# Optimization experiments

Hardware: AMD Instinct MI355X
Metric: run time of the kernel (lower is better)

Reference implementation:

```python
import jax, jax.numpy as jnp
import numpy as np

N_HEADS = 16

def setup_inputs() -> dict:
    key = jax.random.key(0)
    ks = jax.random.split(key, 8)
    B, S, D = 2, 2048, 2048
    H, hd = N_HEADS, D // N_HEADS
    w_scale = 0.02  # keep pre-softmax logits in a sane range
    return {
        "x": jax.random.normal(ks[0], (B, S, D), jnp.float32),
        "Wq": jax.random.normal(ks[1], (D, D), jnp.float32) * w_scale,
        "bq": jax.random.normal(ks[2], (D,), jnp.float32) * w_scale,
        "Wk": jax.random.normal(ks[3], (D, D), jnp.float32) * w_scale,
        "bk": jax.random.normal(ks[4], (D,), jnp.float32) * w_scale,
        "Wv": jax.random.normal(ks[5], (D, D), jnp.float32) * w_scale,
        "bv": jax.random.normal(ks[6], (D,), jnp.float32) * w_scale,
        "k_cache": jnp.zeros((B, H, S, hd), jnp.float32),
        "v_cache": jnp.zeros((B, H, S, hd), jnp.float32),
        "start_pos": 0,
    }

def reference(x, Wq, bq, Wk, bk, Wv, bv, k_cache, v_cache, start_pos):
    B, S, D = x.shape
    H = N_HEADS
    hd = D // H
    # qkv projections (nn.Linear equivalent)
    q_val = (x @ Wq + bq).reshape(B, H, S, hd)  # faithful .view: pure reshape, NO transpose
    k_val = (x @ Wk + bk).reshape(B, H, S, hd)
    v_val = (x @ Wv + bv).reshape(B, H, S, hd)
    # KV-cache scatter update at input_pos = [start_pos, start_pos+S)
    pos = jnp.arange(S) + start_pos
    k_cache = k_cache.at[:, :, pos].set(k_val)
    v_cache = v_cache.at[:, :, pos].set(v_val)
    L = k_cache.shape[2]
    # QK^T / sqrt(hd)
    scores = jnp.einsum('bhsd,bhld->bhsl', q_val, k_cache) / jnp.sqrt(jnp.asarray(hd, x.dtype))
    # default mask path: triu(ones, diag=1) is the KEEP mask (faithful to source)
    mask = jnp.triu(jnp.ones((S, L), x.dtype), 1)
    scores = scores - 1e9 * (1.0 - mask)
    probs = jax.nn.softmax(scores, axis=-1)
    out = jnp.einsum('bhsl,bhld->bhsd', probs, v_cache)  # [B,H,S,hd]
    return out.reshape(B, S, D)  # faithful .view(B, -1, D)
```

## Files before the change

kernel.cpp:

```cpp
#include <hip/hip_runtime.h>
#include <math.h>

#define BATCH 2
#define SEQ   2048
#define DIM   2048
#define NH    16
#define HD    128
#define MTOT  (BATCH*SEQ)
static constexpr float SCALE = 0.08838834764831845f;


typedef short s8  __attribute__((ext_vector_type(8)));
typedef float f4  __attribute__((ext_vector_type(4)));

__device__ inline unsigned short bf_rn(float f) {
    union { float f; unsigned u; } v; v.f = f;
    unsigned r = v.u + 0x7FFFu + ((v.u >> 16) & 1u);
    return (unsigned short)(r >> 16);
}
__device__ inline float bf_f(unsigned short h) {
    union { float f; unsigned u; } v; v.u = ((unsigned)h) << 16; return v.f;
}

#define GLL(g, l) __builtin_amdgcn_global_load_lds( \
    (const __attribute__((address_space(1))) void*)(g), \
    (__attribute__((address_space(3))) void*)(l), 16, 0, 0)

__global__ __launch_bounds__(256) void convert_x(
    const float* __restrict__ x, unsigned short* __restrict__ xh)
{
    size_t i = ((size_t)blockIdx.x * 256 + threadIdx.x) * 4;
    float4 v = *(const float4*)(x + i);
    float a[4] = {v.x, v.y, v.z, v.w};
    ushort4 h;
    unsigned short* hp = &h.x;
    #pragma unroll
    for (int j = 0; j < 4; ++j) hp[j] = bf_rn(a[j]);
    *(ushort4*)(xh + i) = h;
}

__global__ __launch_bounds__(256) void convert_wT(
    const float* __restrict__ Wq, const float* __restrict__ Wk,
    const float* __restrict__ Wv,
    unsigned short* __restrict__ Wth)
{
    const int z = blockIdx.z;
    const float* W = (z == 0) ? Wq : (z == 1) ? Wk : Wv;
    unsigned short* th = Wth + (size_t)z * DIM * DIM;

    __shared__ unsigned short Th[64][72];

    const int k0 = blockIdx.x * 64;
    const int n0 = blockIdx.y * 64;
    const int tid = threadIdx.x;

    #pragma unroll
    for (int i = 0; i < 4; ++i) {
        int idx = tid + i * 256;
        int kk = idx >> 4, n4 = idx & 15;
        float4 w = *(const float4*)(W + (size_t)(k0 + kk) * DIM + n0 + n4 * 4);
        float a[4] = {w.x, w.y, w.z, w.w};
        #pragma unroll
        for (int j = 0; j < 4; ++j)
            Th[n4 * 4 + j][kk] = bf_rn(a[j]);
    }
    __syncthreads();
    #pragma unroll
    for (int i = 0; i < 2; ++i) {
        int idx = tid + i * 256;
        int nn = idx >> 3, c = idx & 7;
        *(uint4*)(th + (size_t)(n0 + nn) * DIM + k0 + c * 8) =
            *(const uint4*)(&Th[nn][c * 8]);
    }
}

__global__ __launch_bounds__(256) void qkv_mfma_split(
    const unsigned short* __restrict__ xh,
    const unsigned short* __restrict__ Wth,
    const float* __restrict__ bq, const float* __restrict__ bk,
    const float* __restrict__ bv,
    unsigned short* __restrict__ qh_, unsigned short* __restrict__ ql_,
    unsigned short* __restrict__ kh_, unsigned short* __restrict__ vh_)
{
    const int z = blockIdx.z;
    const unsigned short* Bhg = Wth + (size_t)z * DIM * DIM;
    const float* bias = (z == 0) ? bq : (z == 1) ? bk : bv;
    unsigned short* dh = (z == 0) ? qh_ : (z == 1) ? kh_ : vh_;
    unsigned short* dl = (z == 0) ? ql_ : (unsigned short*)nullptr;

    const int bm = blockIdx.x * 128;
    const int bn = blockIdx.y * 128;

    __shared__ unsigned short Ah[128 * 32];
    __shared__ unsigned short Bh[128 * 32];

    const int tid = threadIdx.x;
    const int w = tid >> 6, lane = tid & 63;
    const int wr = w >> 1, wc = w & 1;
    const int lr = lane & 15, lg = lane >> 4;

    const int rA0 = bm + (2 * w + 0) * 16 + (lane >> 2);
    const int rA1 = bm + (2 * w + 1) * 16 + (lane >> 2);
    const int rB0 = bn + (2 * w + 0) * 16 + (lane >> 2);
    const int rB1 = bn + (2 * w + 1) * 16 + (lane >> 2);
    const int kin = (lane & 3) * 8;
    const unsigned short* gah0 = xh + (size_t)rA0 * DIM + kin;
    const unsigned short* gah1 = xh + (size_t)rA1 * DIM + kin;
    const unsigned short* gbh0 = Bhg + (size_t)rB0 * DIM + kin;
    const unsigned short* gbh1 = Bhg + (size_t)rB1 * DIM + kin;
    unsigned short* lah0 = &Ah[(2 * w + 0) * 512];
    unsigned short* lah1 = &Ah[(2 * w + 1) * 512];
    unsigned short* lbh0 = &Bh[(2 * w + 0) * 512];
    unsigned short* lbh1 = &Bh[(2 * w + 1) * 512];

    f4 zero4 = {0.f, 0.f, 0.f, 0.f};
    f4 acc[4][4];
    #pragma unroll
    for (int mi = 0; mi < 4; ++mi)
        #pragma unroll
        for (int ni = 0; ni < 4; ++ni) acc[mi][ni] = zero4;

    const unsigned short* pAh = &Ah[(wr * 64 + lr) * 32 + lg * 8];
    const unsigned short* pBh = &Bh[(wc * 64 + lr) * 32 + lg * 8];

    for (int k0 = 0; k0 < DIM; k0 += 32) {
        GLL(gah0 + k0, lah0); GLL(gah1 + k0, lah1);
        GLL(gbh0 + k0, lbh0); GLL(gbh1 + k0, lbh1);
        __syncthreads();

        s8 fah[4], fbh[4];
        #pragma unroll
        for (int i = 0; i < 4; ++i) {
            fah[i] = *(const s8*)(pAh + i * 512);
            fbh[i] = *(const s8*)(pBh + i * 512);
        }
        #pragma unroll
        for (int mi = 0; mi < 4; ++mi)
            #pragma unroll
            for (int ni = 0; ni < 4; ++ni)
                acc[mi][ni] = __builtin_amdgcn_mfma_f32_16x16x32_bf16(
                    fah[mi], fbh[ni], acc[mi][ni], 0, 0, 0);
        __syncthreads();
    }

    float bv_[4]; int col_[4];
    #pragma unroll
    for (int ni = 0; ni < 4; ++ni) {
        col_[ni] = bn + wc * 64 + ni * 16 + lr;
        bv_[ni] = bias[col_[ni]];
    }
    #pragma unroll
    for (int mi = 0; mi < 4; ++mi)
        #pragma unroll
        for (int ni = 0; ni < 4; ++ni)
            #pragma unroll
            for (int r = 0; r < 4; ++r) {
                int row = bm + wr * 64 + mi * 16 + lg * 4 + r;
                float v = acc[mi][ni][r] + bv_[ni];
                size_t idx = (size_t)row * DIM + col_[ni];
                unsigned short h = bf_rn(v);
                dh[idx] = h;
                if (dl) dl[idx] = bf_rn(v - bf_f(h));
            }
}

__global__ __launch_bounds__(256) void transpose_v(
    const unsigned short* __restrict__ vh, unsigned short* __restrict__ vth)
{
    __shared__ unsigned short T[64][72];
    const int s0 = blockIdx.x * 64;
    const int d0 = blockIdx.y * 64;
    const int bh = blockIdx.z;
    const int tid = threadIdx.x;
    {
        const int r = tid >> 2, cs = tid & 3;
        size_t g = ((size_t)bh * SEQ + s0 + r) * HD + d0 + cs * 16;
        *(uint4*)(&T[r][cs * 16])     = *(const uint4*)(vh + g);
        *(uint4*)(&T[r][cs * 16 + 8]) = *(const uint4*)(vh + g + 8);
    }
    __syncthreads();
    {
        const int d = tid >> 2, ss = tid & 3;
        unsigned short bh_[16];
        #pragma unroll
        for (int j = 0; j < 16; ++j)
            bh_[j] = T[ss * 16 + j][d];
        size_t t = ((size_t)bh * HD + d0 + d) * SEQ + s0 + ss * 16;
        *(uint4*)(vth + t)     = ((const uint4*)bh_)[0];
        *(uint4*)(vth + t + 8) = ((const uint4*)bh_)[1];
    }
}

#define KVBLK 32
#define NT    (SEQ / KVBLK)
#define PSTR  40

__global__ __launch_bounds__(256) void attn_mfma(
    const unsigned short* __restrict__ qh, const unsigned short* __restrict__ ql,
    const unsigned short* __restrict__ kh,
    const unsigned short* __restrict__ vth,
    float* __restrict__ out)
{
    __shared__ unsigned short KhA[KVBLK * HD], KhB[KVBLK * HD];
    __shared__ unsigned short VhA[HD * KVBLK], VhB[HD * KVBLK];
    __shared__ unsigned short Ph[4][32 * PSTR];

    const int bid  = blockIdx.x;
    const int slot = bid >> 8;
    const int idx  = bid & 255;
    const int bh_i = idx >> 3;
    const int j    = idx & 7;
    const int qb   = slot ? (14 - j)
                          : (j == 0 ? 0 : (j == 1 ? 15 : j - 1));
    const int h  = bh_i & 15;
    const int b  = bh_i >> 4;
    const int qs = qb * 128;

    const int tid = threadIdx.x;
    const int w = tid >> 6, lane = tid & 63;
    const int lr = lane & 15, lg = lane >> 4;
    const int q0 = w * 32;

    const size_t hbase = (size_t)(b * NH + h) * SEQ * HD;

    s8 fqh[2][4], fql[2][4];
    #pragma unroll
    for (int mi = 0; mi < 2; ++mi)
        #pragma unroll
        for (int k4 = 0; k4 < 4; ++k4) {
            size_t off = hbase + (size_t)(qs + q0 + mi * 16 + lr) * HD
                       + (size_t)((k4 * 4 + lg) * 8);
            fqh[mi][k4] = *(const s8*)(qh + off);
            fql[mi][k4] = *(const s8*)(ql + off);
        }

    s8 ones;
    #pragma unroll
    for (int i = 0; i < 8; ++i) ones[i] = (short)0x3F80;

    f4 O[2][8], Os[2];
    f4 zero4 = {0.f, 0.f, 0.f, 0.f};
    #pragma unroll
    for (int mi = 0; mi < 2; ++mi) {
        #pragma unroll
        for (int nj = 0; nj < 8; ++nj) O[mi][nj] = zero4;
        Os[mi] = zero4;
    }
    float mrun[2][4];
    #pragma unroll
    for (int mi = 0; mi < 2; ++mi)
        #pragma unroll
        for (int r = 0; r < 4; ++r) mrun[mi][r] = -INFINITY;

    const int kr0 = (2 * w + 0) * 4 + (lane >> 4);
    const int kr1 = (2 * w + 1) * 4 + (lane >> 4);
    const int ks  = lane & 15;
    const int vd0 = (2 * w + 0) * 16 + (lane >> 2);
    const int vd1 = (2 * w + 1) * 16 + (lane >> 2);
    const int vs  = lane & 3;
    const size_t kg0 = hbase + (size_t)kr0 * HD + (size_t)((ks ^ (kr0 & 7)) * 8);
    const size_t kg1 = hbase + (size_t)kr1 * HD + (size_t)((ks ^ (kr1 & 7)) * 8);
    const size_t vg0 = hbase + (size_t)vd0 * SEQ + (size_t)((vs ^ (vd0 & 3)) * 8);
    const size_t vg1 = hbase + (size_t)vd1 * SEQ + (size_t)((vs ^ (vd1 & 3)) * 8);

    const int t0 = (qb == 15) ? 0 : qb * 4;

#define STAGE(T_, KH_, VH_) do {                                             \
        const size_t koff = (size_t)(T_) * KVBLK * HD;                       \
        const int    loff = (T_) * KVBLK;                                    \
        GLL(kh + kg0 + koff, &KH_[(2 * w + 0) * 512]);                       \
        GLL(kh + kg1 + koff, &KH_[(2 * w + 1) * 512]);                       \
        GLL(vth + vg0 + loff, &VH_[(2 * w + 0) * 512]);                      \
        GLL(vth + vg1 + loff, &VH_[(2 * w + 1) * 512]);                      \
    } while (0)

    auto compute = [&](int t, const unsigned short* KH, const unsigned short* VH) {
        const int l0 = t * KVBLK;

        s8 fkh[2][4];
        #pragma unroll
        for (int nj = 0; nj < 2; ++nj) {
            const int n = nj * 16 + lr;
            #pragma unroll
            for (int k4 = 0; k4 < 4; ++k4) {
                const int sl = (k4 * 4 + lg) ^ (n & 7);
                fkh[nj][k4] = *(const s8*)(&KH[n * HD + sl * 8]);
            }
        }
        f4 sc[2][2];
        #pragma unroll
        for (int mi = 0; mi < 2; ++mi)
            #pragma unroll
            for (int nj = 0; nj < 2; ++nj) sc[mi][nj] = zero4;
        #pragma unroll
        for (int k4 = 0; k4 < 4; ++k4)
            #pragma unroll
            for (int mi = 0; mi < 2; ++mi)
                #pragma unroll
                for (int nj = 0; nj < 2; ++nj) {
                    sc[mi][nj] = __builtin_amdgcn_mfma_f32_16x16x32_bf16(
                        fqh[mi][k4], fkh[nj][k4], sc[mi][nj], 0, 0, 0);
                    sc[mi][nj] = __builtin_amdgcn_mfma_f32_16x16x32_bf16(
                        fql[mi][k4], fkh[nj][k4], sc[mi][nj], 0, 0, 0);
                }

        float v0[2][4], v1[2][4];
        bool need = false;
        #pragma unroll
        for (int mi = 0; mi < 2; ++mi)
            #pragma unroll
            for (int r = 0; r < 4; ++r) {
                const int srow = qs + q0 + mi * 16 + lg * 4 + r;
                float a = sc[mi][0][r] * SCALE;
                float c = sc[mi][1][r] * SCALE;
                if (l0 + lr      <= srow) a -= 1e9f;
                if (l0 + 16 + lr <= srow) c -= 1e9f;
                v0[mi][r] = a; v1[mi][r] = c;
                const float lim = mrun[mi][r] + 8.f;
                need = need || (a > lim) || (c > lim);
            }

        if (__any(need)) {
            #pragma unroll
            for (int mi = 0; mi < 2; ++mi)
                #pragma unroll
                for (int r = 0; r < 4; ++r) {
                    float rmax = fmaxf(v0[mi][r], v1[mi][r]);
                    #pragma unroll
                    for (int m_ = 1; m_ < 16; m_ <<= 1)
                        rmax = fmaxf(rmax, __shfl_xor(rmax, m_, 64));
                    const float mnew = fmaxf(mrun[mi][r], rmax);
                    const float corr = __expf(mrun[mi][r] - mnew);
                    mrun[mi][r] = mnew;
                    #pragma unroll
                    for (int nj = 0; nj < 8; ++nj) O[mi][nj][r] *= corr;
                    Os[mi][r] *= corr;
                }
        }

        #pragma unroll
        for (int mi = 0; mi < 2; ++mi)
            #pragma unroll
            for (int r = 0; r < 4; ++r) {
                const float p0 = __expf(v0[mi][r] - mrun[mi][r]);
                const float p1 = __expf(v1[mi][r] - mrun[mi][r]);
                const int q = mi * 16 + lg * 4 + r;
                Ph[w][q * PSTR + lr]      = bf_rn(p0);
                Ph[w][q * PSTR + 16 + lr] = bf_rn(p1);
            }

        s8 fph[2], fvh[8];
        #pragma unroll
        for (int mi = 0; mi < 2; ++mi)
            fph[mi] = *(const s8*)(&Ph[w][(mi * 16 + lr) * PSTR + lg * 8]);
        #pragma unroll
        for (int nj = 0; nj < 8; ++nj) {
            const int d = nj * 16 + lr;
            const int sl = lg ^ (d & 3);
            fvh[nj] = *(const s8*)(&VH[d * KVBLK + sl * 8]);
        }
        #pragma unroll
        for (int mi = 0; mi < 2; ++mi) {
            #pragma unroll
            for (int nj = 0; nj < 8; ++nj)
                O[mi][nj] = __builtin_amdgcn_mfma_f32_16x16x32_bf16(
                    fph[mi], fvh[nj], O[mi][nj], 0, 0, 0);
            Os[mi] = __builtin_amdgcn_mfma_f32_16x16x32_bf16(
                fph[mi], ones, Os[mi], 0, 0, 0);
        }
    };

    STAGE(t0, KhA, VhA);
    __syncthreads();
    for (int t = t0; t < NT; t += 2) {
        STAGE(t + 1, KhB, VhB);
        compute(t, KhA, VhA);
        __syncthreads();
        if (t + 2 < NT) STAGE(t + 2, KhA, VhA);
        compute(t + 1, KhB, VhB);
        __syncthreads();
    }
#undef STAGE

    float* op = out + hbase;
    float inv[2][4];
    #pragma unroll
    for (int mi = 0; mi < 2; ++mi)
        #pragma unroll
        for (int r = 0; r < 4; ++r) inv[mi][r] = 1.f / Os[mi][r];
    #pragma unroll
    for (int mi = 0; mi < 2; ++mi)
        #pragma unroll
        for (int nj = 0; nj < 8; ++nj)
            #pragma unroll
            for (int r = 0; r < 4; ++r) {
                const int srow = qs + q0 + mi * 16 + lg * 4 + r;
                op[(size_t)srow * HD + nj * 16 + lr] = O[mi][nj][r] * inv[mi][r];
            }
}

__global__ __launch_bounds__(256) void qkv_gemm(
    const float* __restrict__ x,
    const float* __restrict__ Wq, const float* __restrict__ bq,
    const float* __restrict__ Wk, const float* __restrict__ bk,
    const float* __restrict__ Wv, const float* __restrict__ bv,
    float* __restrict__ Qo, float* __restrict__ Ko, float* __restrict__ Vo)
{
    const int z = blockIdx.z;
    const float* W    = (z == 0) ? Wq : (z == 1) ? Wk : Wv;
    const float* bias = (z == 0) ? bq : (z == 1) ? bk : bv;
    float*       dst  = (z == 0) ? Qo : (z == 1) ? Ko : Vo;

    __shared__ float As[32][64];
    __shared__ float Bs[32][64];

    const int row0 = blockIdx.x * 64;
    const int col0 = blockIdx.y * 64;
    const int tid  = threadIdx.x;
    const int tm   = tid >> 4;
    const int tn   = tid & 15;

    float acc[4][4] = {};

    for (int k0 = 0; k0 < DIM; k0 += 32) {
        #pragma unroll
        for (int i = 0; i < 2; ++i) {
            int f = tid + i * 256;
            int r = f >> 3, c4 = f & 7;
            float4 a = *(const float4*)(x + (size_t)(row0 + r) * DIM + k0 + c4 * 4);
            As[c4 * 4 + 0][r] = a.x;
            As[c4 * 4 + 1][r] = a.y;
            As[c4 * 4 + 2][r] = a.z;
            As[c4 * 4 + 3][r] = a.w;
        }
        #pragma unroll
        for (int i = 0; i < 2; ++i) {
            int f = tid + i * 256;
            int r = f >> 4, c4 = f & 15;
            *(float4*)(&Bs[r][c4 * 4]) =
                *(const float4*)(W + (size_t)(k0 + r) * DIM + col0 + c4 * 4);
        }
        __syncthreads();
        #pragma unroll
        for (int k = 0; k < 32; ++k) {
            float4 a4 = *(const float4*)(&As[k][tm * 4]);
            float4 b4 = *(const float4*)(&Bs[k][tn * 4]);
            float av[4] = {a4.x, a4.y, a4.z, a4.w};
            float bw[4] = {b4.x, b4.y, b4.z, b4.w};
            #pragma unroll
            for (int i = 0; i < 4; ++i)
                #pragma unroll
                for (int j2 = 0; j2 < 4; ++j2)
                    acc[i][j2] += av[i] * bw[j2];
        }
        __syncthreads();
    }

    float4 bb = *(const float4*)(bias + col0 + tn * 4);
    float bsv[4] = {bb.x, bb.y, bb.z, bb.w};
    #pragma unroll
    for (int i = 0; i < 4; ++i) {
        int r = row0 + tm * 4 + i;
        float4 o;
        o.x = acc[i][0] + bsv[0];
        o.y = acc[i][1] + bsv[1];
        o.z = acc[i][2] + bsv[2];
        o.w = acc[i][3] + bsv[3];
        *(float4*)(dst + (size_t)r * DIM + col0 + tn * 4) = o;
    }
}

__global__ __launch_bounds__(256) void attn_kernel(
    const float* Qbuf,
    const float* __restrict__ Kc,
    const float* __restrict__ Vc,
    float* Out)
{
    __shared__ float smem[16384];
    float* QsT = smem;
    float* Ks  = smem + 8192;
    float* Ps  = smem + 8192;

    const int bid = blockIdx.x;
    const int qb  = bid & 31;
    const int h   = (bid >> 5) & 15;
    const int b   = bid >> 9;
    const size_t base = (size_t)b * SEQ * DIM + (size_t)h * SEQ * HD;
    const float* Qp = Qbuf + base;
    const float* Kp = Kc + base;
    const float* Vp = Vc + base;
    float*       Op = Out + base;

    const int tid = threadIdx.x;
    const int tm  = tid >> 4;
    const int tn  = tid & 15;
    const int qs  = qb * 64;

    #pragma unroll
    for (int i = 0; i < 8; ++i) {
        int f = tid + i * 256;
        int r = f >> 5, c4 = f & 31;
        float4 q = *(const float4*)(Qp + (size_t)(qs + r) * HD + c4 * 4);
        QsT[(c4 * 4 + 0) * 64 + r] = q.x;
        QsT[(c4 * 4 + 1) * 64 + r] = q.y;
        QsT[(c4 * 4 + 2) * 64 + r] = q.z;
        QsT[(c4 * 4 + 3) * 64 + r] = q.w;
    }

    float O[4][8] = {};
    float mrun[4], lrun[4];
    #pragma unroll
    for (int i = 0; i < 4; ++i) { mrun[i] = -INFINITY; lrun[i] = 0.f; }

    const int t0 = (qb == 31) ? 0 : qb;

    __syncthreads();

    for (int t = t0; t < 32; ++t) {
        const int l0 = t * 64;

        #pragma unroll
        for (int i = 0; i < 8; ++i) {
            int f = tid + i * 256;
            int r = f >> 5, c4 = f & 31;
            float4 kv = *(const float4*)(Kp + (size_t)(l0 + r) * HD + c4 * 4);
            int sc4 = c4 ^ ((r >> 2) & 7);
            *(float4*)(&Ks[r * 128 + sc4 * 4]) = kv;
        }
        __syncthreads();

        float sc[4][4] = {};
        for (int k4 = 0; k4 < 32; ++k4) {
            const int kb = k4 * 4;
            float qv[4][4];
            #pragma unroll
            for (int kk = 0; kk < 4; ++kk) {
                float4 q = *(const float4*)(&QsT[(kb + kk) * 64 + tm * 4]);
                qv[kk][0] = q.x; qv[kk][1] = q.y; qv[kk][2] = q.z; qv[kk][3] = q.w;
            }
            float kvv[4][4];
            #pragma unroll
            for (int j = 0; j < 4; ++j) {
                const int n = tn * 4 + j;
                float4 kv = *(const float4*)(&Ks[n * 128 + ((k4 ^ (tn & 7)) << 2)]);
                kvv[j][0] = kv.x; kvv[j][1] = kv.y; kvv[j][2] = kv.z; kvv[j][3] = kv.w;
            }
            #pragma unroll
            for (int kk = 0; kk < 4; ++kk)
                #pragma unroll
                for (int i = 0; i < 4; ++i)
                    #pragma unroll
                    for (int j = 0; j < 4; ++j)
                        sc[i][j] += qv[kk][i] * kvv[j][kk];
        }

        #pragma unroll
        for (int i = 0; i < 4; ++i) {
            const int srow = qs + tm * 4 + i;
            #pragma unroll
            for (int j = 0; j < 4; ++j) {
                float v = sc[i][j] * SCALE;
                const int l = l0 + tn * 4 + j;
                if (l <= srow) v -= 1e9f;
                sc[i][j] = v;
            }
        }

        float corr[4], rsum[4];
        #pragma unroll
        for (int i = 0; i < 4; ++i) {
            float rmax = fmaxf(fmaxf(sc[i][0], sc[i][1]), fmaxf(sc[i][2], sc[i][3]));
            #pragma unroll
            for (int off = 1; off < 16; off <<= 1)
                rmax = fmaxf(rmax, __shfl_xor(rmax, off, 64));
            const float mnew = fmaxf(mrun[i], rmax);
            corr[i] = __expf(mrun[i] - mnew);
            mrun[i] = mnew;
            float s = 0.f;
            #pragma unroll
            for (int j = 0; j < 4; ++j) {
                const float p = __expf(sc[i][j] - mnew);
                sc[i][j] = p;
                s += p;
            }
            #pragma unroll
            for (int off = 1; off < 16; off <<= 1)
                s += __shfl_xor(s, off, 64);
            rsum[i] = s;
        }
        #pragma unroll
        for (int i = 0; i < 4; ++i) {
            lrun[i] = lrun[i] * corr[i] + rsum[i];
            #pragma unroll
            for (int d = 0; d < 8; ++d) O[i][d] *= corr[i];
        }

        __syncthreads();

        #pragma unroll
        for (int i = 0; i < 4; ++i) {
            float4 p4 = make_float4(sc[i][0], sc[i][1], sc[i][2], sc[i][3]);
            *(float4*)(&Ps[(tm * 4 + i) * 68 + tn * 4]) = p4;
        }
        __syncthreads();

        for (int n4 = 0; n4 < 16; ++n4) {
            float pa[4][4];
            #pragma unroll
            for (int i = 0; i < 4; ++i) {
                float4 p = *(const float4*)(&Ps[(tm * 4 + i) * 68 + n4 * 4]);
                pa[i][0] = p.x; pa[i][1] = p.y; pa[i][2] = p.z; pa[i][3] = p.w;
            }
            #pragma unroll
            for (int nn = 0; nn < 4; ++nn) {
                const int l = l0 + n4 * 4 + nn;
                const float4 v0 = *(const float4*)(Vp + (size_t)l * HD + tn * 8);
                const float4 v1 = *(const float4*)(Vp + (size_t)l * HD + tn * 8 + 4);
                #pragma unroll
                for (int i = 0; i < 4; ++i) {
                    const float p = pa[i][nn];
                    O[i][0] += p * v0.x; O[i][1] += p * v0.y;
                    O[i][2] += p * v0.z; O[i][3] += p * v0.w;
                    O[i][4] += p * v1.x; O[i][5] += p * v1.y;
                    O[i][6] += p * v1.z; O[i][7] += p * v1.w;
                }
            }
        }
        __syncthreads();
    }

    #pragma unroll
    for (int i = 0; i < 4; ++i) {
        const float inv = 1.f / lrun[i];
        const int r = qs + tm * 4 + i;
        float4 o0 = make_float4(O[i][0] * inv, O[i][1] * inv, O[i][2] * inv, O[i][3] * inv);
        float4 o1 = make_float4(O[i][4] * inv, O[i][5] * inv, O[i][6] * inv, O[i][7] * inv);
        *(float4*)(Op + (size_t)r * HD + tn * 8)     = o0;
        *(float4*)(Op + (size_t)r * HD + tn * 8 + 4) = o1;
    }
}

extern "C" void kernel_launch(void* const* d_in, const int* in_sizes, int n_in,
                              void* d_out, int out_size, void* d_ws, size_t ws_size,
                              hipStream_t stream) {
    const float* x  = (const float*)d_in[0];
    const float* Wq = (const float*)d_in[1];
    const float* bq = (const float*)d_in[2];
    const float* Wk = (const float*)d_in[3];
    const float* bk = (const float*)d_in[4];
    const float* Wv = (const float*)d_in[5];
    const float* bv = (const float*)d_in[6];

    float* out = (float*)d_out;

    const size_t NM = (size_t)MTOT * DIM;
    const size_t DD = (size_t)DIM * DIM;

    const size_t NEED2 = NM * 16 + DD * 6;

    if (ws_size >= NEED2) {
        unsigned short* xh  = (unsigned short*)d_ws;
        unsigned short* xl  = xh + NM;
        unsigned short* Wth = xl + NM;
        unsigned short* qh_ = Wth + 3 * DD;
        unsigned short* ql_ = qh_ + NM;
        unsigned short* kh_ = ql_ + NM;
        unsigned short* kl_ = kh_ + NM;
        unsigned short* vh_ = kl_ + NM;
        unsigned short* vth = xh;

        convert_x<<<dim3((unsigned)(NM / 4 / 256)), 256, 0, stream>>>(x, xh);
        convert_wT<<<dim3(32, 32, 3), 256, 0, stream>>>(Wq, Wk, Wv, Wth);
        qkv_mfma_split<<<dim3(MTOT / 128, DIM / 128, 3), 256, 0, stream>>>(
            xh, Wth, bq, bk, bv, qh_, ql_, kh_, vh_);
        transpose_v<<<dim3(SEQ / 64, HD / 64, BATCH * NH), 256, 0, stream>>>(
            vh_, vth);
        attn_mfma<<<dim3(BATCH * NH * (SEQ / 128)), 256, 0, stream>>>(
            qh_, ql_, kh_, vth, out);
    } else {
        float* Kbuf = (float*)d_ws;
        float* Vbuf = Kbuf + NM;
        qkv_gemm<<<dim3(MTOT / 64, DIM / 64, 3), 256, 0, stream>>>(
            x, Wq, bq, Wk, bk, Wv, bv, out, Kbuf, Vbuf);
        attn_kernel<<<dim3(BATCH * NH * (SEQ / 64)), 256, 0, stream>>>(
            out, Kbuf, Vbuf, out);
    }
}
```

Before: 265.0 us.

## Drop Q low-part split and fold softmax scale and log2e into Q projection

Removes the bf16 hi/lo split of Q, so the QK^T inner loop issues half as many MFMAs and the projection no longer writes, and attention no longer loads, the ql buffer. The softmax scale and log2(e) are folded into the Q projection epilogue, which lets the attention kernel use exp2 directly and drop the per-score multiply; the mask constant and rescale threshold are adjusted to the log2 domain. This trades some precision in the logits (Q now rounded to bf16 once, after scaling) for less compute and memory traffic.

Measured after the change: 264.9 us. No clear change (-0.0%).

```diff
diff --git a/kernel.cpp b/kernel.cpp
--- a/kernel.cpp
+++ b/kernel.cpp
@@ -7,7 +7,10 @@
 #define NH    16
 #define HD    128
 #define MTOT  (BATCH*SEQ)
-static constexpr float SCALE = 0.08838834764831845f;
+static constexpr float SCALE  = 0.08838834764831845f;
+static constexpr float L2E    = 1.4426950408889634f;
+static constexpr float QSCALE = SCALE * L2E;
+static constexpr float MASKC  = 1.0e9f * L2E;
 
 
 typedef short s8  __attribute__((ext_vector_type(8)));
@@ -17,9 +20,6 @@
     union { float f; unsigned u; } v; v.f = f;
     unsigned r = v.u + 0x7FFFu + ((v.u >> 16) & 1u);
     return (unsigned short)(r >> 16);
-}
-__device__ inline float bf_f(unsigned short h) {
-    union { float f; unsigned u; } v; v.u = ((unsigned)h) << 16; return v.f;
 }
 
 #define GLL(g, l) __builtin_amdgcn_global_load_lds( \
@@ -79,14 +79,14 @@
     const unsigned short* __restrict__ Wth,
     const float* __restrict__ bq, const float* __restrict__ bk,
     const float* __restrict__ bv,
-    unsigned short* __restrict__ qh_, unsigned short* __restrict__ ql_,
-    unsigned short* __restrict__ kh_, unsigned short* __restrict__ vh_)
+    unsigned short* __restrict__ qh_, unsigned short* __restrict__ kh_,
+    unsigned short* __restrict__ vh_)
 {
     const int z = blockIdx.z;
     const unsigned short* Bhg = Wth + (size_t)z * DIM * DIM;
     const float* bias = (z == 0) ? bq : (z == 1) ? bk : bv;
     unsigned short* dh = (z == 0) ? qh_ : (z == 1) ? kh_ : vh_;
-    unsigned short* dl = (z == 0) ? ql_ : (unsigned short*)nullptr;
+    const float oscale = (z == 0) ? QSCALE : 1.0f;
 
     const int bm = blockIdx.x * 128;
     const int bn = blockIdx.y * 128;
@@ -156,11 +156,8 @@
             #pragma unroll
             for (int r = 0; r < 4; ++r) {
                 int row = bm + wr * 64 + mi * 16 + lg * 4 + r;
-                float v = acc[mi][ni][r] + bv_[ni];
-                size_t idx = (size_t)row * DIM + col_[ni];
-                unsigned short h = bf_rn(v);
-                dh[idx] = h;
-                if (dl) dl[idx] = bf_rn(v - bf_f(h));
+                float v = (acc[mi][ni][r] + bv_[ni]) * oscale;
+                dh[(size_t)row * DIM + col_[ni]] = bf_rn(v);
             }
 }
 
@@ -196,7 +193,7 @@
 #define PSTR  40
 
 __global__ __launch_bounds__(256) void attn_mfma(
-    const unsigned short* __restrict__ qh, const unsigned short* __restrict__ ql,
+    const unsigned short* __restrict__ qh,
     const unsigned short* __restrict__ kh,
     const unsigned short* __restrict__ vth,
     float* __restrict__ out)
@@ -223,7 +220,7 @@
 
     const size_t hbase = (size_t)(b * NH + h) * SEQ * HD;
 
-    s8 fqh[2][4], fql[2][4];
+    s8 fqh[2][4];
     #pragma unroll
     for (int mi = 0; mi < 2; ++mi)
         #pragma unroll
@@ -231,7 +228,6 @@
             size_t off = hbase + (size_t)(qs + q0 + mi * 16 + lr) * HD
                        + (size_t)((k4 * 4 + lg) * 8);
             fqh[mi][k4] = *(const s8*)(qh + off);
-            fql[mi][k4] = *(const s8*)(ql + off);
         }
 
     s8 ones;
@@ -297,12 +293,9 @@
             #pragma unroll
             for (int mi = 0; mi < 2; ++mi)
                 #pragma unroll
-                for (int nj = 0; nj < 2; ++nj) {
+                for (int nj = 0; nj < 2; ++nj)
                     sc[mi][nj] = __builtin_amdgcn_mfma_f32_16x16x32_bf16(
                         fqh[mi][k4], fkh[nj][k4], sc[mi][nj], 0, 0, 0);
-                    sc[mi][nj] = __builtin_amdgcn_mfma_f32_16x16x32_bf16(
-                        fql[mi][k4], fkh[nj][k4], sc[mi][nj], 0, 0, 0);
-                }
 
         float v0[2][4], v1[2][4];
         bool need = false;
@@ -311,12 +304,12 @@
             #pragma unroll
             for (int r = 0; r < 4; ++r) {
                 const int srow = qs + q0 + mi * 16 + lg * 4 + r;
-                float a = sc[mi][0][r] * SCALE;
-                float c = sc[mi][1][r] * SCALE;
-                if (l0 + lr      <= srow) a -= 1e9f;
-                if (l0 + 16 + lr <= srow) c -= 1e9f;
+                float a = sc[mi][0][r];
+                float c = sc[mi][1][r];
+                if (l0 + lr      <= srow) a -= MASKC;
+                if (l0 + 16 + lr <= srow) c -= MASKC;
                 v0[mi][r] = a; v1[mi][r] = c;
-                const float lim = mrun[mi][r] + 8.f;
+                const float lim = mrun[mi][r] + 11.5f;
                 need = need || (a > lim) || (c > lim);
             }
 
@@ -330,7 +323,7 @@
                     for (int m_ = 1; m_ < 16; m_ <<= 1)
                         rmax = fmaxf(rmax, __shfl_xor(rmax, m_, 64));
                     const float mnew = fmaxf(mrun[mi][r], rmax);
-                    const float corr = __expf(mrun[mi][r] - mnew);
+                    const float corr = exp2f(mrun[mi][r] - mnew);
                     mrun[mi][r] = mnew;
                     #pragma unroll
                     for (int nj = 0; nj < 8; ++nj) O[mi][nj][r] *= corr;
@@ -342,8 +335,8 @@
         for (int mi = 0; mi < 2; ++mi)
             #pragma unroll
             for (int r = 0; r < 4; ++r) {
-                const float p0 = __expf(v0[mi][r] - mrun[mi][r]);
-                const float p1 = __expf(v1[mi][r] - mrun[mi][r]);
+                const float p0 = exp2f(v0[mi][r] - mrun[mi][r]);
+                const float p1 = exp2f(v1[mi][r] - mrun[mi][r]);
                 const int q = mi * 16 + lg * 4 + r;
                 Ph[w][q * PSTR + lr]      = bf_rn(p0);
                 Ph[w][q * PSTR + 16 + lr] = bf_rn(p1);
@@ -672,11 +665,11 @@
         convert_x<<<dim3((unsigned)(NM / 4 / 256)), 256, 0, stream>>>(x, xh);
         convert_wT<<<dim3(32, 32, 3), 256, 0, stream>>>(Wq, Wk, Wv, Wth);
         qkv_mfma_split<<<dim3(MTOT / 128, DIM / 128, 3), 256, 0, stream>>>(
-            xh, Wth, bq, bk, bv, qh_, ql_, kh_, vh_);
+            xh, Wth, bq, bk, bv, qh_, kh_, vh_);
         transpose_v<<<dim3(SEQ / 64, HD / 64, BATCH * NH), 256, 0, stream>>>(
             vh_, vth);
         attn_mfma<<<dim3(BATCH * NH * (SEQ / 128)), 256, 0, stream>>>(
-            qh_, ql_, kh_, vth, out);
+            qh_, kh_, vth, out);
     } else {
         float* Kbuf = (float*)d_ws;
         float* Vbuf = Kbuf + NM;
```
